# Optimization experiments

Hardware: AMD Instinct MI355X
Metric: run time of the kernel (lower is better)

## Reference

```python
import jax, jax.numpy as jnp
import numpy as np

B, LQ, NB, NT = 4, 512, 32, 256
D_MODEL, N_HEADS, D_K, D_V = 512, 8, 64, 64
SCALE = 1.0 / np.sqrt(D_K).astype(np.float32)


def setup_inputs() -> dict:
    key = jax.random.key(0)
    ks = jax.random.split(key, 16)
    std = 0.02
    p = lambda k, shp: (std * jax.random.normal(k, shp, dtype=jnp.float32))
    return {
        'q':   jax.random.normal(ks[0], (B, LQ, D_MODEL), dtype=jnp.float32),
        'k_w': jax.random.normal(ks[1], (B, NB, NT, D_MODEL), dtype=jnp.float32),
        'v_w': jax.random.normal(ks[2], (B, NB, NT, D_MODEL), dtype=jnp.float32),
        'k_s': jax.random.normal(ks[3], (B, NB, D_MODEL), dtype=jnp.float32),
        'v_s': jax.random.normal(ks[4], (B, NB, D_MODEL), dtype=jnp.float32),
        'W_qs': p(ks[5], (D_MODEL, N_HEADS * D_K)), 'b_qs': jnp.zeros((N_HEADS * D_K,), jnp.float32),
        'W_ks': p(ks[6], (D_MODEL, N_HEADS * D_K)), 'b_ks': jnp.zeros((N_HEADS * D_K,), jnp.float32),
        'W_vs': p(ks[7], (D_MODEL, N_HEADS * D_V)), 'b_vs': jnp.zeros((N_HEADS * D_V,), jnp.float32),
        'W_qw': p(ks[8], (D_MODEL, N_HEADS * D_K)), 'b_qw': jnp.zeros((N_HEADS * D_K,), jnp.float32),
        'W_kw': p(ks[9], (D_MODEL, N_HEADS * D_K)), 'b_kw': jnp.zeros((N_HEADS * D_K,), jnp.float32),
        'W_vw': p(ks[10], (D_MODEL, N_HEADS * D_V)), 'b_vw': jnp.zeros((N_HEADS * D_V,), jnp.float32),
        'W_fc1': p(ks[11], (N_HEADS * D_V, D_MODEL)), 'b_fc1': jnp.zeros((D_MODEL,), jnp.float32),
        'W_fc':  p(ks[12], (D_MODEL + N_HEADS * D_V, D_MODEL)), 'b_fc': jnp.zeros((D_MODEL,), jnp.float32),
    }


def reference(q, k_w, v_w, k_s, v_s,
              W_qs, b_qs, W_ks, b_ks, W_vs, b_vs,
              W_qw, b_qw, W_kw, b_kw, W_vw, b_vw,
              W_fc1, b_fc1, W_fc, b_fc):
    b, lq = q.shape[0], q.shape[1]
    nb, nt = k_w.shape[1], k_w.shape[2]
    h, dk, dv = N_HEADS, D_K, D_V

    # ---- sentence-level (graph) attention ----
    qs = (q @ W_qs + b_qs).reshape(b, lq, h, dk)        # [b,lq,h,dk]
    ks_ = (k_s @ W_ks + b_ks).reshape(b, nb, h, dk)     # [b,nb,h,dk]
    vs_ = (v_s @ W_vs + b_vs).reshape(b, nb, h, dv)     # [b,nb,h,dv]
    attn_s = jnp.einsum('bqhd,bnhd->bhqn', qs * SCALE, ks_)  # [b,h,lq,nb]
    attn_s = jax.nn.softmax(attn_s, axis=-1)
    ctx_s = jnp.einsum('bhqn,bnhd->bqhd', attn_s, vs_).reshape(b, lq, h * dv)
    ctx_s = ctx_s @ W_fc1 + b_fc1                        # [b,lq,d_model]

    # ---- token-level attention with sentence norm ----
    qw = (q @ W_qw + b_qw).reshape(b, lq, h, dk)         # [b,lq,h,dk]
    kw = (k_w @ W_kw + b_kw).reshape(b, nb, nt, h, dk)
    vw = (v_w @ W_vw + b_vw).reshape(b, nb, nt, h, dv)
    attn_w = jnp.einsum('bqhd,bnthd->bhqnt', qw * SCALE, kw)  # [b,h,lq,nb,nt]
    wts = jax.nn.softmax(attn_w, axis=-1)                # softmax over tokens within each block
    aw = wts * attn_s[..., None]                         # sentence-weighted token attention
    ctx_w = jnp.einsum('bhqnt,bnthd->bqhd', aw, vw).reshape(b, lq, h * dv)

    out = jnp.concatenate([ctx_s, ctx_w], axis=-1) @ W_fc + b_fc  # [b,lq,d_model]
    return out
```

## Files before the change

kernel.cpp:

```cpp
#include <hip/hip_runtime.h>
#include <hip/hip_bf16.h>

#define SCALE_F 0.125f

typedef __attribute__((ext_vector_type(8))) short short8;
typedef __attribute__((ext_vector_type(4))) float f32x4;

__device__ __forceinline__ unsigned short f2b(float f){
  return __builtin_bit_cast(unsigned short, __float2bfloat16(f));
}
__device__ __forceinline__ float b2f(unsigned short h){
  return __uint_as_float((unsigned int)h << 16);
}

__global__ __launch_bounds__(256)
void wcast_t(const float* __restrict__ W0, unsigned short* __restrict__ T0,
             const float* __restrict__ W1, unsigned short* __restrict__ T1)
{
  __shared__ unsigned short tile[64][72];
  const float* W = blockIdx.z ? W1 : W0;
  unsigned short* T = blockIdx.z ? T1 : T0;
  int k0 = blockIdx.x * 64, n0 = blockIdx.y * 64;
  #pragma unroll
  for (int j = 0; j < 16; j++) {
    int idx = threadIdx.x + j * 256;
    int r = idx >> 6, c = idx & 63;
    tile[r][c] = f2b(W[(size_t)(k0 + r) * 512 + n0 + c]);
  }
  __syncthreads();
  #pragma unroll
  for (int j = 0; j < 16; j++) {
    int idx = threadIdx.x + j * 256;
    int r = idx >> 6, c = idx & 63;
    T[(size_t)(n0 + r) * 512 + k0 + c] = tile[c][r];
  }
}

template<int MODE>
__device__ __forceinline__ void sgemm_body(
    unsigned short* sm, const float* __restrict__ A,
    const float* __restrict__ p0, const float* __restrict__ p1,
    const float* __restrict__ W, const float* __restrict__ bias,
    float* __restrict__ outf, float scale, int m0, int n0, int K, int tid)
{
  unsigned short* Ah = sm;
  unsigned short* Al = sm + 4096;
  unsigned short* Bh = sm + 8192;
  unsigned short* Bl = sm + 12288;
  const int lane = tid & 63, wv = tid >> 6, lr = lane & 15, lg = lane >> 4;

  f32x4 acc[4];
  #pragma unroll
  for (int nf = 0; nf < 4; nf++) acc[nf] = (f32x4){0.f, 0.f, 0.f, 0.f};

  for (int k0 = 0; k0 < K; k0 += 64) {
    float4 a0[2], a1[2];
    float bw[2][8];
    const bool dual = (MODE == 1) && (k0 >= 512);
    const int kk = dual ? (k0 - 512) : k0;
    #pragma unroll
    for (int j = 0; j < 2; j++) {
      int idx = tid + j * 256;
      int row = idx >> 3, c8 = idx & 7;
      size_t base = (size_t)(m0 + row) * 512 + kk + c8 * 8;
      if (dual) {
        float4 x0 = *(const float4*)&p0[base];
        float4 x1 = *(const float4*)&p0[base + 4];
        float4 y0 = *(const float4*)&p1[base];
        float4 y1 = *(const float4*)&p1[base + 4];
        a0[j] = (float4){x0.x + y0.x, x0.y + y0.y, x0.z + y0.z, x0.w + y0.w};
        a1[j] = (float4){x1.x + y1.x, x1.y + y1.y, x1.z + y1.z, x1.w + y1.w};
      } else {
        a0[j] = *(const float4*)&A[base];
        a1[j] = *(const float4*)&A[base + 4];
      }
    }
    #pragma unroll
    for (int j = 0; j < 2; j++) {
      int idx = tid + j * 256;
      int nl = idx >> 3, kseg = idx & 7;
      #pragma unroll
      for (int e = 0; e < 8; e++)
        bw[j][e] = W[(size_t)(k0 + kseg * 8 + e) * 512 + n0 + nl];
    }
    __syncthreads();
    #pragma unroll
    for (int j = 0; j < 2; j++) {
      int idx = tid + j * 256;
      int row = idx >> 3, c8 = idx & 7;
      int off = row * 64 + ((c8 * 8) ^ ((row & 7) << 3));
      float v[8] = {a0[j].x, a0[j].y, a0[j].z, a0[j].w,
                    a1[j].x, a1[j].y, a1[j].z, a1[j].w};
      short8 h, l;
      #pragma unroll
      for (int e = 0; e < 8; e++) {
        unsigned short hh = f2b(v[e]);
        h[e] = (short)hh;
        l[e] = (short)f2b(v[e] - b2f(hh));
      }
      *(short8*)&Ah[off] = h;
      *(short8*)&Al[off] = l;
    }
    #pragma unroll
    for (int j = 0; j < 2; j++) {
      int idx = tid + j * 256;
      int nl = idx >> 3, kseg = idx & 7;
      int off = nl * 64 + ((kseg * 8) ^ ((nl & 7) << 3));
      short8 h, l;
      #pragma unroll
      for (int e = 0; e < 8; e++) {
        unsigned short hh = f2b(bw[j][e]);
        h[e] = (short)hh;
        l[e] = (short)f2b(bw[j][e] - b2f(hh));
      }
      *(short8*)&Bh[off] = h;
      *(short8*)&Bl[off] = l;
    }
    __syncthreads();
    #pragma unroll
    for (int ks = 0; ks < 2; ks++) {
      int rowa = wv * 16 + lr;
      int aoff = rowa * 64 + ((ks * 32 + lg * 8) ^ ((rowa & 7) << 3));
      short8 ah = *(const short8*)&Ah[aoff];
      short8 al = *(const short8*)&Al[aoff];
      #pragma unroll
      for (int nf = 0; nf < 4; nf++) {
        int rowb = nf * 16 + lr;
        int boff = rowb * 64 + ((ks * 32 + lg * 8) ^ ((rowb & 7) << 3));
        short8 bh = *(const short8*)&Bh[boff];
        short8 bl = *(const short8*)&Bl[boff];
        acc[nf] = __builtin_amdgcn_mfma_f32_16x16x32_bf16(ah, bh, acc[nf], 0, 0, 0);
        acc[nf] = __builtin_amdgcn_mfma_f32_16x16x32_bf16(ah, bl, acc[nf], 0, 0, 0);
        acc[nf] = __builtin_amdgcn_mfma_f32_16x16x32_bf16(al, bh, acc[nf], 0, 0, 0);
      }
    }
  }

  #pragma unroll
  for (int nf = 0; nf < 4; nf++) {
    int n = n0 + nf * 16 + lr;
    float bv = bias[n];
    #pragma unroll
    for (int i = 0; i < 4; i++) {
      int m = m0 + wv * 16 + lg * 4 + i;
      float v = (acc[nf][i] + bv) * scale;
      if (MODE == 0 || MODE == 1) {
        outf[(size_t)m * 512 + n] = v;
      } else if (MODE == 2) {
        int bb = m >> 9, qq = m & 511, hh = n >> 6, d = n & 63;
        outf[((((size_t)bb * 8 + hh) * 512 + qq) << 6) + d] = v;
      } else {
        int bb = m >> 5, nn = m & 31, hh = n >> 6, d = n & 63;
        outf[((((size_t)bb * 8 + hh) * 32 + nn) << 6) + d] = v;
      }
    }
  }
}

template<int VT>
__device__ __forceinline__ void proj_body(
    unsigned short* sm, const float* __restrict__ A,
    const unsigned short* __restrict__ BT, const float* __restrict__ bias,
    __hip_bfloat16* __restrict__ outW, int bidLocal, int tid)
{
  unsigned short* As = sm;
  unsigned short* Bs = sm + 8192;
  const int xcd = bidLocal & 7, local = bidLocal >> 3;
  const int mx = xcd * 32 + (local >> 2);
  const int ny = local & 3;
  const int m0 = mx * 128, n0 = ny * 128;
  const int lane = tid & 63, wv = tid >> 6, lr = lane & 15, lg = lane >> 4;
  const int wr = wv >> 1, wc = wv & 1;

  f32x4 acc[4][4];
  #pragma unroll
  for (int mi = 0; mi < 4; mi++)
    #pragma unroll
    for (int nj = 0; nj < 4; nj++) acc[mi][nj] = (f32x4){0.f, 0.f, 0.f, 0.f};

  for (int k0 = 0; k0 < 512; k0 += 64) {
    float4 a0[4], a1[4]; uint4 bq[4];
    #pragma unroll
    for (int j = 0; j < 4; j++) {
      int idx = tid + j * 256;
      int row = idx >> 3, c8 = idx & 7;
      const float* ap = A + (size_t)(m0 + row) * 512 + k0 + c8 * 8;
      a0[j] = *(const float4*)ap;
      a1[j] = *(const float4*)(ap + 4);
      bq[j] = *(const uint4*)(BT + (size_t)(n0 + row) * 512 + k0 + c8 * 8);
    }
    __syncthreads();
    #pragma unroll
    for (int j = 0; j < 4; j++) {
      int idx = tid + j * 256;
      int row = idx >> 3, c8 = idx & 7;
      int off = row * 64 + ((c8 * 8) ^ ((row & 7) << 3));
      short8 pk;
      pk[0] = (short)f2b(a0[j].x); pk[1] = (short)f2b(a0[j].y);
      pk[2] = (short)f2b(a0[j].z); pk[3] = (short)f2b(a0[j].w);
      pk[4] = (short)f2b(a1[j].x); pk[5] = (short)f2b(a1[j].y);
      pk[6] = (short)f2b(a1[j].z); pk[7] = (short)f2b(a1[j].w);
      *(short8*)&As[off] = pk;
      *(uint4*)&Bs[off] = bq[j];
    }
    __syncthreads();
    #pragma unroll
    for (int ks = 0; ks < 2; ks++) {
      short8 af[4], bfp[4];
      #pragma unroll
      for (int mi = 0; mi < 4; mi++) {
        int row = wr * 64 + mi * 16 + lr;
        af[mi] = *(const short8*)&As[row * 64 + ((ks * 32 + lg * 8) ^ ((row & 7) << 3))];
      }
      #pragma unroll
      for (int nj = 0; nj < 4; nj++) {
        int row = wc * 64 + nj * 16 + lr;
        bfp[nj] = *(const short8*)&Bs[row * 64 + ((ks * 32 + lg * 8) ^ ((row & 7) << 3))];
      }
      #pragma unroll
      for (int mi = 0; mi < 4; mi++)
        #pragma unroll
        for (int nj = 0; nj < 4; nj++)
          acc[mi][nj] = __builtin_amdgcn_mfma_f32_16x16x32_bf16(af[mi], bfp[nj], acc[mi][nj], 0, 0, 0);
    }
  }

  #pragma unroll
  for (int nj = 0; nj < 4; nj++) {
    int n = n0 + wc * 64 + nj * 16 + lr;
    float bv = bias[n];
    int hh = n >> 6, d = n & 63;
    #pragma unroll
    for (int mi = 0; mi < 4; mi++) {
      if (VT == 0) {
        #pragma unroll
        for (int i = 0; i < 4; i++) {
          int m = m0 + wr * 64 + mi * 16 + lg * 4 + i;
          int bb = m >> 13, r = m & 8191, nn = r >> 8, tt = r & 255;
          outW[(((((size_t)bb * 8 + hh) * 32 + nn) * 256 + tt) << 6) + d] =
              __float2bfloat16(acc[mi][nj][i] + bv);
        }
      } else {
        int m = m0 + wr * 64 + mi * 16 + lg * 4;
        int bb = m >> 13, r = m & 8191, nn = r >> 8, t0 = r & 255;
        uint2 pk;
        pk.x = (unsigned)f2b(acc[mi][nj][0] + bv) | ((unsigned)f2b(acc[mi][nj][1] + bv) << 16);
        pk.y = (unsigned)f2b(acc[mi][nj][2] + bv) | ((unsigned)f2b(acc[mi][nj][3] + bv) << 16);
        *(uint2*)((unsigned short*)outW +
                  (((((size_t)bb * 8 + hh) * 32 + nn) * 64 + d) << 8) + t0) = pk;
      }
    }
  }
}

__device__ __forceinline__ void tok_body(
    unsigned short* sm, const float* __restrict__ qw,
    const __hip_bfloat16* __restrict__ kw, const __hip_bfloat16* __restrict__ vwT,
    const float* __restrict__ attn_s, float* __restrict__ part0,
    float* __restrict__ part1, int bid, int tid)
{
  unsigned short* kvbuf = sm;
  unsigned short* pbuf  = sm + 18432;
  const int xcd = bid & 7, slot = bid >> 3;
  const int bh = xcd * 4 + (slot >> 4);
  const int rest = slot & 15;
  const int qt = rest >> 1, z = rest & 1;
  const int b = bh >> 3, h = bh & 7;
  const int wv = tid >> 6, lane = tid & 63, lg = lane >> 4, lr = lane & 15;
  const int qbase = qt * 64 + wv * 16;
  const int n0 = z * 16;
  const int vd = wv * 16 + (lane >> 2), tq = lane & 3;

  short8 qfrag[2];
  {
    const float* qrow = qw + ((size_t)bh * 512 + qbase + lr) * 64;
    #pragma unroll
    for (int ks = 0; ks < 2; ks++) {
      float4 u0 = *(const float4*)&qrow[ks * 32 + lg * 8];
      float4 u1 = *(const float4*)&qrow[ks * 32 + lg * 8 + 4];
      short8 t;
      t[0] = f2b(u0.x); t[1] = f2b(u0.y); t[2] = f2b(u0.z); t[3] = f2b(u0.w);
      t[4] = f2b(u1.x); t[5] = f2b(u1.y); t[6] = f2b(u1.z); t[7] = f2b(u1.w);
      qfrag[ks] = t;
    }
  }
  float asv[16];
  {
    const float* ap = attn_s + ((size_t)bh * 512 + qbase + lr) * 32 + n0;
    #pragma unroll
    for (int i = 0; i < 4; i++) {
      float4 u = *(const float4*)&ap[i * 4];
      asv[i * 4 + 0] = u.x; asv[i * 4 + 1] = u.y;
      asv[i * 4 + 2] = u.z; asv[i * 4 + 3] = u.w;
    }
  }

  f32x4 acc[4];
  #pragma unroll
  for (int dt = 0; dt < 4; dt++) acc[dt] = (f32x4){0.f, 0.f, 0.f, 0.f};

  const unsigned short* kwb = (const unsigned short*)kw + (size_t)bh * 32 * 256 * 64;
  const unsigned short* vtb = (const unsigned short*)vwT + (size_t)bh * 32 * 64 * 256;
  const unsigned int pbase = (wv * 16 + lr) * 264;

  for (int ni = 0; ni < 16; ni++) {
    const int n = n0 + ni;
    __syncthreads();
    {
      const unsigned short* ksrc = kwb + ((size_t)n * 256 + tid) * 64;
      uint4 r[8];
      #pragma unroll
      for (int j = 0; j < 8; j++) r[j] = *(const uint4*)(ksrc + j * 8);
      #pragma unroll
      for (int j = 0; j < 8; j++) *(uint4*)&kvbuf[tid * 72 + j * 8] = r[j];
    }
    __syncthreads();

    f32x4 sfr[16];
    #pragma unroll
    for (int tt = 0; tt < 16; tt++) sfr[tt] = (f32x4){0.f, 0.f, 0.f, 0.f};
    __builtin_amdgcn_s_setprio(1);
    #pragma unroll
    for (int tt = 0; tt < 16; tt++) {
      #pragma unroll
      for (int ks = 0; ks < 2; ks++) {
        short8 kf = *(const short8*)&kvbuf[(16 * tt + lr) * 72 + ks * 32 + lg * 8];
        sfr[tt] = __builtin_amdgcn_mfma_f32_16x16x32_bf16(kf, qfrag[ks], sfr[tt], 0, 0, 0);
      }
    }
    __builtin_amdgcn_s_setprio(0);
    float lsum = 0.f;
    #pragma unroll
    for (int tt = 0; tt < 16; tt++) {
      #pragma unroll
      for (int i = 0; i < 4; i++) {
        float e = __expf(sfr[tt][i]);
        sfr[tt][i] = e;
        lsum += e;
      }
    }
    lsum += __shfl_xor(lsum, 16);
    lsum += __shfl_xor(lsum, 32);
    const float coef = asv[ni] / lsum;
    #pragma unroll
    for (int tt = 0; tt < 16; tt++) {
      uint2 pk;
      pk.x = (unsigned)f2b(sfr[tt][0] * coef) | ((unsigned)f2b(sfr[tt][1] * coef) << 16);
      pk.y = (unsigned)f2b(sfr[tt][2] * coef) | ((unsigned)f2b(sfr[tt][3] * coef) << 16);
      *(uint2*)&pbuf[pbase + tt * 16 + lg * 4] = pk;
    }
    __syncthreads();

    {
      const unsigned short* vsrc = vtb + ((size_t)n * 64 + vd) * 256 + tq * 64;
      uint4 r[8];
      #pragma unroll
      for (int j = 0; j < 8; j++) r[j] = *(const uint4*)(vsrc + j * 8);
      #pragma unroll
      for (int j = 0; j < 8; j++)
        *(uint4*)&kvbuf[vd * 264 + tq * 64 + ((j ^ tq) * 8)] = r[j];
    }
    __syncthreads();

    __builtin_amdgcn_s_setprio(1);
    #pragma unroll
    for (int ks = 0; ks < 8; ks++) {
      short8 pa = *(const short8*)&pbuf[pbase + ks * 32 + lg * 8];
      const int tqe = ks >> 1, joff = (ks & 1) * 4 + lg;
      #pragma unroll
      for (int dt = 0; dt < 4; dt++) {
        short8 vb = *(const short8*)&kvbuf[(16 * dt + lr) * 264 + tqe * 64 + ((joff ^ tqe) * 8)];
        acc[dt] = __builtin_amdgcn_mfma_f32_16x16x32_bf16(pa, vb, acc[dt], 0, 0, 0);
      }
    }
    __builtin_amdgcn_s_setprio(0);
  }

  float* pout = z ? part1 : part0;
  #pragma unroll
  for (int dt = 0; dt < 4; dt++) {
    #pragma unroll
    for (int i = 0; i < 4; i++) {
      int qg = qt * 64 + wv * 16 + lg * 4 + i;
      pout[((size_t)b * 512 + qg) * 512 + h * 64 + dt * 16 + lr] = acc[dt][i];
    }
  }
}

__global__ __launch_bounds__(256)
void megaA(const float* __restrict__ q,
           const float* __restrict__ k_w, const float* __restrict__ v_w,
           const float* __restrict__ k_s, const float* __restrict__ v_s,
           const float* __restrict__ W_qs, const float* __restrict__ b_qs,
           const float* __restrict__ W_qw, const float* __restrict__ b_qw,
           const float* __restrict__ W_ks, const float* __restrict__ b_ks,
           const float* __restrict__ W_vs, const float* __restrict__ b_vs,
           const unsigned short* __restrict__ WkT, const float* __restrict__ b_kw,
           const unsigned short* __restrict__ WvT, const float* __restrict__ b_vw,
           float* qs_ws, float* qw_ws, float* ks_ws, float* vs_ws,
           __hip_bfloat16* kw_ws, __hip_bfloat16* vwT_ws)
{
  __shared__ unsigned short sm[16384];
  const int bid = blockIdx.x, tid = threadIdx.x;
  if (bid < 1024) {
    proj_body<0>(sm, k_w, WkT, b_kw, kw_ws, bid, tid);
  } else if (bid < 2048) {
    proj_body<1>(sm, v_w, WvT, b_vw, vwT_ws, bid - 1024, tid);
  } else if (bid < 2560) {
    int local = bid - 2048;
    int bx = local & 31, by = (local >> 5) & 7, bz = local >> 8;
    if (bz == 0)
      sgemm_body<2>(sm, q, nullptr, nullptr, W_qs, b_qs, qs_ws, SCALE_F, bx * 64, by * 64, 512, tid);
    else
      sgemm_body<2>(sm, q, nullptr, nullptr, W_qw, b_qw, qw_ws, SCALE_F, bx * 64, by * 64, 512, tid);
  } else {
    int local = bid - 2560;
    int bx = local & 1, by = (local >> 1) & 7, bz = local >> 4;
    if (bz == 0)
      sgemm_body<3>(sm, k_s, nullptr, nullptr, W_ks, b_ks, ks_ws, 1.f, bx * 64, by * 64, 512, tid);
    else
      sgemm_body<3>(sm, v_s, nullptr, nullptr, W_vs, b_vs, vs_ws, 1.f, bx * 64, by * 64, 512, tid);
  }
}

__global__ __launch_bounds__(256, 2)
void megaB(const float* __restrict__ qw,
           const __hip_bfloat16* __restrict__ kw, const __hip_bfloat16* __restrict__ vwT,
           const float* __restrict__ attn_s, float* part0, float* part1,
           const float* __restrict__ ctxs,
           const float* __restrict__ W_fc1, const float* __restrict__ b_fc1,
           float* ctxsf)
{
  __shared__ unsigned short sm[35328];
  const int bid = blockIdx.x, tid = threadIdx.x;
  if (bid < 512) {
    tok_body(sm, qw, kw, vwT, attn_s, part0, part1, bid, tid);
  } else {
    int local = bid - 512;
    sgemm_body<0>(sm, ctxs, nullptr, nullptr, W_fc1, b_fc1, ctxsf, 1.f,
                  (local & 31) * 64, (local >> 5) * 64, 512, tid);
  }
}

__global__ __launch_bounds__(256)
void final_gemm(const float* __restrict__ ctxsf,
                const float* __restrict__ p0, const float* __restrict__ p1,
                const float* __restrict__ W, const float* __restrict__ bias,
                float* out)
{
  __shared__ unsigned short sm[16384];
  sgemm_body<1>(sm, ctxsf, p0, p1, W, bias, out, 1.f,
                blockIdx.x * 64, blockIdx.y * 64, 1024, threadIdx.x);
}

__global__ __launch_bounds__(256)
void sent_attn(const float* __restrict__ qs,
               const float* __restrict__ ks,
               const float* __restrict__ vs,
               float* __restrict__ attn_s,
               float* __restrict__ ctx_s)
{
  __shared__ float qsS[32][68];
  __shared__ float ksS[32][68];
  __shared__ float vsS[32][68];
  __shared__ float sS[32][36];
  const int bh = blockIdx.y, b = bh >> 3, h = bh & 7;
  const int q0 = blockIdx.x * 32;
  const int tid = threadIdx.x;

  #pragma unroll
  for (int i = 0; i < 2; i++) {
    int idx = tid + i * 256;
    int r = idx >> 4, c = (idx & 15) * 4;
    *(float4*)&qsS[r][c] = *(const float4*)&qs[((size_t)bh * 512 + q0 + r) * 64 + c];
    *(float4*)&ksS[r][c] = *(const float4*)&ks[((size_t)bh * 32 + r) * 64 + c];
    *(float4*)&vsS[r][c] = *(const float4*)&vs[((size_t)bh * 32 + r) * 64 + c];
  }
  __syncthreads();

  #pragma unroll
  for (int it = 0; it < 4; it++) {
    int pair = tid + it * 256;
    int qq = pair >> 5, nn = pair & 31;
    float s = 0.f;
    #pragma unroll
    for (int k = 0; k < 64; k++) s += qsS[qq][k] * ksS[nn][k];
    sS[qq][nn] = s;
  }
  __syncthreads();

  if (tid < 32) {
    int qq = tid;
    float m = -1e30f;
    #pragma unroll
    for (int n = 0; n < 32; n++) m = fmaxf(m, sS[qq][n]);
    float p[32];
    float sum = 0.f;
    #pragma unroll
    for (int n = 0; n < 32; n++) { p[n] = __expf(sS[qq][n] - m); sum += p[n]; }
    float inv = 1.f / sum;
    #pragma unroll
    for (int n = 0; n < 32; n++) {
      float pv = p[n] * inv;
      sS[qq][n] = pv;
      attn_s[((size_t)bh * 512 + q0 + qq) * 32 + n] = pv;
    }
  }
  __syncthreads();

  #pragma unroll
  for (int it = 0; it < 8; it++) {
    int idx = tid + it * 256;
    int qq = idx >> 6, d = idx & 63;
    float c = 0.f;
    #pragma unroll
    for (int n = 0; n < 32; n++) c += sS[qq][n] * vsS[n][d];
    ctx_s[((size_t)b * 512 + q0 + qq) * 512 + h * 64 + d] = c;
  }
}

extern "C" void kernel_launch(void* const* d_in, const int* in_sizes, int n_in,
                              void* d_out, int out_size, void* d_ws, size_t ws_size,
                              hipStream_t stream)
{
  (void)in_sizes; (void)n_in; (void)out_size; (void)ws_size;
  const float* q    = (const float*)d_in[0];
  const float* k_w  = (const float*)d_in[1];
  const float* v_w  = (const float*)d_in[2];
  const float* k_s  = (const float*)d_in[3];
  const float* v_s  = (const float*)d_in[4];
  const float* W_qs = (const float*)d_in[5];  const float* b_qs = (const float*)d_in[6];
  const float* W_ks = (const float*)d_in[7];  const float* b_ks = (const float*)d_in[8];
  const float* W_vs = (const float*)d_in[9];  const float* b_vs = (const float*)d_in[10];
  const float* W_qw = (const float*)d_in[11]; const float* b_qw = (const float*)d_in[12];
  const float* W_kw = (const float*)d_in[13]; const float* b_kw = (const float*)d_in[14];
  const float* W_vw = (const float*)d_in[15]; const float* b_vw = (const float*)d_in[16];
  const float* W_fc1= (const float*)d_in[17]; const float* b_fc1= (const float*)d_in[18];
  const float* W_fc = (const float*)d_in[19]; const float* b_fc = (const float*)d_in[20];
  float* out = (float*)d_out;

  char* ws = (char*)d_ws;
  const size_t MB = 1ull << 20;
  const size_t KB = 1ull << 10;
  float* qs_ws    = (float*)(ws + 0 * MB);
  float* qw_ws    = (float*)(ws + 4 * MB);
  float* ks_ws    = (float*)(ws + 8 * MB);
  unsigned short* WkT = (unsigned short*)(ws + 8 * MB + 512 * KB);
  float* vs_ws    = (float*)(ws + 9 * MB);
  unsigned short* WvT = (unsigned short*)(ws + 9 * MB + 512 * KB);
  float* attns_ws = (float*)(ws + 10 * MB);
  float* ctxs_ws  = (float*)(ws + 12 * MB);
  float* ctxsf_ws = (float*)(ws + 16 * MB);
  float* part1    = (float*)(ws + 20 * MB);
  __hip_bfloat16* kw_ws  = (__hip_bfloat16*)(ws + 24 * MB);
  __hip_bfloat16* vwT_ws = (__hip_bfloat16*)(ws + 56 * MB);
  float* part0    = (float*)(ws + 0 * MB);

  dim3 blk(256);
  wcast_t<<<dim3(8, 8, 2), blk, 0, stream>>>(W_kw, WkT, W_vw, WvT);
  megaA<<<dim3(2592), blk, 0, stream>>>(
      q, k_w, v_w, k_s, v_s,
      W_qs, b_qs, W_qw, b_qw, W_ks, b_ks, W_vs, b_vs,
      WkT, b_kw, WvT, b_vw,
      qs_ws, qw_ws, ks_ws, vs_ws, kw_ws, vwT_ws);
  sent_attn<<<dim3(16, 32), blk, 0, stream>>>(qs_ws, ks_ws, vs_ws, attns_ws, ctxs_ws);
  megaB<<<dim3(768), blk, 0, stream>>>(
      qw_ws, kw_ws, vwT_ws, attns_ws, part0, part1,
      ctxs_ws, W_fc1, b_fc1, ctxsf_ws);
  final_gemm<<<dim3(32, 8), blk, 0, stream>>>(ctxsf_ws, part0, part1, W_fc, b_fc, out);
}
```

Before: 287.2 us.

## Pre-cast k_w/v_w to bf16 and stage projection tiles via global_load_lds

Adds a prep kernel that converts the large fp32 k_w and v_w tensors to bf16 in workspace, alongside the existing weight transpose-cast. The k/v projection GEMM then loads bf16 tiles straight into swizzled LDS with global_load_lds, skipping the register round-trip and in-loop conversion. The path is chosen only when the workspace holds at least 152 MB, otherwise the old register-staged path runs. It costs an extra full read and write of both 32 MB inputs and still has no double buffering, since it waits on vmcnt(0) every k-step.

```diff
diff --git a/kernel.cpp b/kernel.cpp
--- a/kernel.cpp
+++ b/kernel.cpp
@@ -5,35 +5,14 @@
 
 typedef __attribute__((ext_vector_type(8))) short short8;
 typedef __attribute__((ext_vector_type(4))) float f32x4;
+typedef __attribute__((address_space(3))) void lds_void;
+typedef const __attribute__((address_space(1))) void glb_void;
 
 __device__ __forceinline__ unsigned short f2b(float f){
   return __builtin_bit_cast(unsigned short, __float2bfloat16(f));
 }
 __device__ __forceinline__ float b2f(unsigned short h){
   return __uint_as_float((unsigned int)h << 16);
-}
-
-__global__ __launch_bounds__(256)
-void wcast_t(const float* __restrict__ W0, unsigned short* __restrict__ T0,
-             const float* __restrict__ W1, unsigned short* __restrict__ T1)
-{
-  __shared__ unsigned short tile[64][72];
-  const float* W = blockIdx.z ? W1 : W0;
-  unsigned short* T = blockIdx.z ? T1 : T0;
-  int k0 = blockIdx.x * 64, n0 = blockIdx.y * 64;
-  #pragma unroll
-  for (int j = 0; j < 16; j++) {
-    int idx = threadIdx.x + j * 256;
-    int r = idx >> 6, c = idx & 63;
-    tile[r][c] = f2b(W[(size_t)(k0 + r) * 512 + n0 + c]);
-  }
-  __syncthreads();
-  #pragma unroll
-  for (int j = 0; j < 16; j++) {
-    int idx = threadIdx.x + j * 256;
-    int r = idx >> 6, c = idx & 63;
-    T[(size_t)(n0 + r) * 512 + k0 + c] = tile[c][r];
-  }
 }
 
 template<int MODE>
@@ -158,73 +137,11 @@
 }
 
 template<int VT>
-__device__ __forceinline__ void proj_body(
-    unsigned short* sm, const float* __restrict__ A,
-    const unsigned short* __restrict__ BT, const float* __restrict__ bias,
-    __hip_bfloat16* __restrict__ outW, int bidLocal, int tid)
-{
-  unsigned short* As = sm;
-  unsigned short* Bs = sm + 8192;
-  const int xcd = bidLocal & 7, local = bidLocal >> 3;
-  const int mx = xcd * 32 + (local >> 2);
-  const int ny = local & 3;
-  const int m0 = mx * 128, n0 = ny * 128;
-  const int lane = tid & 63, wv = tid >> 6, lr = lane & 15, lg = lane >> 4;
-  const int wr = wv >> 1, wc = wv & 1;
-
-  f32x4 acc[4][4];
-  #pragma unroll
-  for (int mi = 0; mi < 4; mi++)
-    #pragma unroll
-    for (int nj = 0; nj < 4; nj++) acc[mi][nj] = (f32x4){0.f, 0.f, 0.f, 0.f};
-
-  for (int k0 = 0; k0 < 512; k0 += 64) {
-    float4 a0[4], a1[4]; uint4 bq[4];
-    #pragma unroll
-    for (int j = 0; j < 4; j++) {
-      int idx = tid + j * 256;
-      int row = idx >> 3, c8 = idx & 7;
-      const float* ap = A + (size_t)(m0 + row) * 512 + k0 + c8 * 8;
-      a0[j] = *(const float4*)ap;
-      a1[j] = *(const float4*)(ap + 4);
-      bq[j] = *(const uint4*)(BT + (size_t)(n0 + row) * 512 + k0 + c8 * 8);
-    }
-    __syncthreads();
-    #pragma unroll
-    for (int j = 0; j < 4; j++) {
-      int idx = tid + j * 256;
-      int row = idx >> 3, c8 = idx & 7;
-      int off = row * 64 + ((c8 * 8) ^ ((row & 7) << 3));
-      short8 pk;
-      pk[0] = (short)f2b(a0[j].x); pk[1] = (short)f2b(a0[j].y);
-      pk[2] = (short)f2b(a0[j].z); pk[3] = (short)f2b(a0[j].w);
-      pk[4] = (short)f2b(a1[j].x); pk[5] = (short)f2b(a1[j].y);
-      pk[6] = (short)f2b(a1[j].z); pk[7] = (short)f2b(a1[j].w);
-      *(short8*)&As[off] = pk;
-      *(uint4*)&Bs[off] = bq[j];
-    }
-    __syncthreads();
-    #pragma unroll
-    for (int ks = 0; ks < 2; ks++) {
-      short8 af[4], bfp[4];
-      #pragma unroll
-      for (int mi = 0; mi < 4; mi++) {
-        int row = wr * 64 + mi * 16 + lr;
-        af[mi] = *(const short8*)&As[row * 64 + ((ks * 32 + lg * 8) ^ ((row & 7) << 3))];
-      }
-      #pragma unroll
-      for (int nj = 0; nj < 4; nj++) {
-        int row = wc * 64 + nj * 16 + lr;
-        bfp[nj] = *(const short8*)&Bs[row * 64 + ((ks * 32 + lg * 8) ^ ((row & 7) << 3))];
-      }
-      #pragma unroll
-      for (int mi = 0; mi < 4; mi++)
-        #pragma unroll
-        for (int nj = 0; nj < 4; nj++)
-          acc[mi][nj] = __builtin_amdgcn_mfma_f32_16x16x32_bf16(af[mi], bfp[nj], acc[mi][nj], 0, 0, 0);
-    }
-  }
-
+__device__ __forceinline__ void proj_epilogue(
+    f32x4 (&acc)[4][4], const float* __restrict__ bias,
+    __hip_bfloat16* __restrict__ outW, int m0, int n0,
+    int wr, int wc, int lr, int lg)
+{
   #pragma unroll
   for (int nj = 0; nj < 4; nj++) {
     int n = n0 + wc * 64 + nj * 16 + lr;
@@ -253,6 +170,136 @@
   }
 }
 
+template<int VT>
+__device__ __forceinline__ void proj_reg(
+    unsigned short* sm, const float* __restrict__ A,
+    const unsigned short* __restrict__ BT, const float* __restrict__ bias,
+    __hip_bfloat16* __restrict__ outW, int bidLocal, int tid)
+{
+  unsigned short* As = sm;
+  unsigned short* Bs = sm + 8192;
+  const int xcd = bidLocal & 7, local = bidLocal >> 3;
+  const int mx = xcd * 32 + (local >> 2);
+  const int ny = local & 3;
+  const int m0 = mx * 128, n0 = ny * 128;
+  const int lane = tid & 63, wv = tid >> 6, lr = lane & 15, lg = lane >> 4;
+  const int wr = wv >> 1, wc = wv & 1;
+
+  f32x4 acc[4][4];
+  #pragma unroll
+  for (int mi = 0; mi < 4; mi++)
+    #pragma unroll
+    for (int nj = 0; nj < 4; nj++) acc[mi][nj] = (f32x4){0.f, 0.f, 0.f, 0.f};
+
+  for (int k0 = 0; k0 < 512; k0 += 64) {
+    float4 a0[4], a1[4]; uint4 bq[4];
+    #pragma unroll
+    for (int j = 0; j < 4; j++) {
+      int idx = tid + j * 256;
+      int row = idx >> 3, c8 = idx & 7;
+      const float* ap = A + (size_t)(m0 + row) * 512 + k0 + c8 * 8;
+      a0[j] = *(const float4*)ap;
+      a1[j] = *(const float4*)(ap + 4);
+      bq[j] = *(const uint4*)(BT + (size_t)(n0 + row) * 512 + k0 + c8 * 8);
+    }
+    __syncthreads();
+    #pragma unroll
+    for (int j = 0; j < 4; j++) {
+      int idx = tid + j * 256;
+      int row = idx >> 3, c8 = idx & 7;
+      int off = row * 64 + ((c8 * 8) ^ ((row & 7) << 3));
+      short8 pk;
+      pk[0] = (short)f2b(a0[j].x); pk[1] = (short)f2b(a0[j].y);
+      pk[2] = (short)f2b(a0[j].z); pk[3] = (short)f2b(a0[j].w);
+      pk[4] = (short)f2b(a1[j].x); pk[5] = (short)f2b(a1[j].y);
+      pk[6] = (short)f2b(a1[j].z); pk[7] = (short)f2b(a1[j].w);
+      *(short8*)&As[off] = pk;
+      *(uint4*)&Bs[off] = bq[j];
+    }
+    __syncthreads();
+    #pragma unroll
+    for (int ks = 0; ks < 2; ks++) {
+      short8 af[4], bfp[4];
+      #pragma unroll
+      for (int mi = 0; mi < 4; mi++) {
+        int row = wr * 64 + mi * 16 + lr;
+        af[mi] = *(const short8*)&As[row * 64 + ((ks * 32 + lg * 8) ^ ((row & 7) << 3))];
+      }
+      #pragma unroll
+      for (int nj = 0; nj < 4; nj++) {
+        int row = wc * 64 + nj * 16 + lr;
+        bfp[nj] = *(const short8*)&Bs[row * 64 + ((ks * 32 + lg * 8) ^ ((row & 7) << 3))];
+      }
+      #pragma unroll
+      for (int mi = 0; mi < 4; mi++)
+        #pragma unroll
+        for (int nj = 0; nj < 4; nj++)
+          acc[mi][nj] = __builtin_amdgcn_mfma_f32_16x16x32_bf16(af[mi], bfp[nj], acc[mi][nj], 0, 0, 0);
+    }
+  }
+  proj_epilogue<VT>(acc, bias, outW, m0, n0, wr, wc, lr, lg);
+}
+
+template<int VT>
+__device__ __forceinline__ void proj_glds(
+    unsigned short* sm, const unsigned short* __restrict__ Abf,
+    const unsigned short* __restrict__ BT, const float* __restrict__ bias,
+    __hip_bfloat16* __restrict__ outW, int bidLocal, int tid)
+{
+  unsigned short* As = sm;
+  unsigned short* Bs = sm + 8192;
+  const int xcd = bidLocal & 7, local = bidLocal >> 3;
+  const int mx = xcd * 32 + (local >> 2);
+  const int ny = local & 3;
+  const int m0 = mx * 128, n0 = ny * 128;
+  const int lane = tid & 63, wv = tid >> 6, lr = lane & 15, lg = lane >> 4;
+  const int wr = wv >> 1, wc = wv & 1;
+  const int srow = tid >> 3, scc = tid & 7;
+
+  f32x4 acc[4][4];
+  #pragma unroll
+  for (int mi = 0; mi < 4; mi++)
+    #pragma unroll
+    for (int nj = 0; nj < 4; nj++) acc[mi][nj] = (f32x4){0.f, 0.f, 0.f, 0.f};
+
+  for (int k0 = 0; k0 < 512; k0 += 64) {
+    __syncthreads();
+    #pragma unroll
+    for (int issue = 0; issue < 4; issue++) {
+      int row = issue * 32 + srow;
+      int cs = (scc ^ (row & 7)) * 8;
+      const unsigned short* ga = Abf + (size_t)(m0 + row) * 512 + k0 + cs;
+      const unsigned short* gb = BT  + (size_t)(n0 + row) * 512 + k0 + cs;
+      unsigned short* la = As + issue * 2048 + wv * 512;
+      unsigned short* lb = Bs + issue * 2048 + wv * 512;
+      __builtin_amdgcn_global_load_lds((glb_void*)ga, (lds_void*)la, 16, 0, 0);
+      __builtin_amdgcn_global_load_lds((glb_void*)gb, (lds_void*)lb, 16, 0, 0);
+    }
+    asm volatile("s_waitcnt vmcnt(0)" ::: "memory");
+    __syncthreads();
+    #pragma unroll
+    for (int ks = 0; ks < 2; ks++) {
+      short8 af[4], bfp[4];
+      #pragma unroll
+      for (int mi = 0; mi < 4; mi++) {
+        int row = wr * 64 + mi * 16 + lr;
+        af[mi] = *(const short8*)&As[row * 64 + ((ks * 32 + lg * 8) ^ ((row & 7) << 3))];
+      }
+      #pragma unroll
+      for (int nj = 0; nj < 4; nj++) {
+        int row = wc * 64 + nj * 16 + lr;
+        bfp[nj] = *(const short8*)&Bs[row * 64 + ((ks * 32 + lg * 8) ^ ((row & 7) << 3))];
+      }
+      #pragma unroll
+      for (int mi = 0; mi < 4; mi++)
+        #pragma unroll
+        for (int nj = 0; nj < 4; nj++)
+          acc[mi][nj] = __builtin_amdgcn_mfma_f32_16x16x32_bf16(af[mi], bfp[nj], acc[mi][nj], 0, 0, 0);
+    }
+  }
+  proj_epilogue<VT>(acc, bias, outW, m0, n0, wr, wc, lr, lg);
+}
+
 __device__ __forceinline__ void tok_body(
     unsigned short* sm, const float* __restrict__ qw,
     const __hip_bfloat16* __restrict__ kw, const __hip_bfloat16* __restrict__ vwT,
@@ -388,8 +435,51 @@
 }
 
 __global__ __launch_bounds__(256)
-void megaA(const float* __restrict__ q,
-           const float* __restrict__ k_w, const float* __restrict__ v_w,
+void prep(const float* __restrict__ kwf, const float* __restrict__ vwf,
+          unsigned short* __restrict__ kbf, unsigned short* __restrict__ vbf,
+          const float* __restrict__ W0, unsigned short* __restrict__ T0,
+          const float* __restrict__ W1, unsigned short* __restrict__ T1,
+          int ncast)
+{
+  __shared__ unsigned short tile[64][72];
+  const int bid = blockIdx.x, tid = threadIdx.x;
+  if (bid < 2 * ncast) {
+    const float* src = (bid < ncast) ? kwf : vwf;
+    unsigned short* dst = (bid < ncast) ? kbf : vbf;
+    size_t off = (size_t)((bid < ncast) ? bid : bid - ncast) * 8192;
+    #pragma unroll
+    for (int i = 0; i < 8; i++) {
+      size_t idx = off + ((size_t)i * 256 + tid) * 4;
+      float4 v = *(const float4*)&src[idx];
+      uint2 pk;
+      pk.x = (unsigned)f2b(v.x) | ((unsigned)f2b(v.y) << 16);
+      pk.y = (unsigned)f2b(v.z) | ((unsigned)f2b(v.w) << 16);
+      *(uint2*)&dst[idx] = pk;
+    }
+  } else {
+    int local = bid - 2 * ncast;
+    const float* W = (local >> 6) ? W1 : W0;
+    unsigned short* T = (local >> 6) ? T1 : T0;
+    int k0 = (local & 7) * 64, n0 = ((local >> 3) & 7) * 64;
+    #pragma unroll
+    for (int j = 0; j < 16; j++) {
+      int idx = tid + j * 256;
+      int r = idx >> 6, c = idx & 63;
+      tile[r][c] = f2b(W[(size_t)(k0 + r) * 512 + n0 + c]);
+    }
+    __syncthreads();
+    #pragma unroll
+    for (int j = 0; j < 16; j++) {
+      int idx = tid + j * 256;
+      int r = idx >> 6, c = idx & 63;
+      T[(size_t)(n0 + r) * 512 + k0 + c] = tile[c][r];
+    }
+  }
+}
+
+__global__ __launch_bounds__(256)
+void megaA_glds(const float* __restrict__ q,
+           const unsigned short* __restrict__ kbf, const unsigned short* __restrict__ vbf,
            const float* __restrict__ k_s, const float* __restrict__ v_s,
            const float* __restrict__ W_qs, const float* __restrict__ b_qs,
            const float* __restrict__ W_qw, const float* __restrict__ b_qw,
@@ -403,9 +493,9 @@
   __shared__ unsigned short sm[16384];
   const int bid = blockIdx.x, tid = threadIdx.x;
   if (bid < 1024) {
-    proj_body<0>(sm, k_w, WkT, b_kw, kw_ws, bid, tid);
+    proj_glds<0>(sm, kbf, WkT, b_kw, kw_ws, bid, tid);
   } else if (bid < 2048) {
-    proj_body<1>(sm, v_w, WvT, b_vw, vwT_ws, bid - 1024, tid);
+    proj_glds<1>(sm, vbf, WvT, b_vw, vwT_ws, bid - 1024, tid);
   } else if (bid < 2560) {
     int local = bid - 2048;
     int bx = local & 31, by = (local >> 5) & 7, bz = local >> 8;
@@ -423,6 +513,42 @@
   }
 }
 
+__global__ __launch_bounds__(256)
+void megaA_reg(const float* __restrict__ q,
+           const float* __restrict__ k_w, const float* __restrict__ v_w,
+           const float* __restrict__ k_s, const float* __restrict__ v_s,
+           const float* __restrict__ W_qs, const float* __restrict__ b_qs,
+           const float* __restrict__ W_qw, const float* __restrict__ b_qw,
+           const float* __restrict__ W_ks, const float* __restrict__ b_ks,
+           const float* __restrict__ W_vs, const float* __restrict__ b_vs,
+           const unsigned short* __restrict__ WkT, const float* __restrict__ b_kw,
+           const unsigned short* __restrict__ WvT, const float* __restrict__ b_vw,
+           float* qs_ws, float* qw_ws, float* ks_ws, float* vs_ws,
+           __hip_bfloat16* kw_ws, __hip_bfloat16* vwT_ws)
+{
+  __shared__ unsigned short sm[16384];
+  const int bid = blockIdx.x, tid = threadIdx.x;
+  if (bid < 1024) {
+    proj_reg<0>(sm, k_w, WkT, b_kw, kw_ws, bid, tid);
+  } else if (bid < 2048) {
+    proj_reg<1>(sm, v_w, WvT, b_vw, vwT_ws, bid - 1024, tid);
+  } else if (bid < 2560) {
+    int local = bid - 2048;
+    int bx = local & 31, by = (local >> 5) & 7, bz = local >> 8;
+    if (bz == 0)
+      sgemm_body<2>(sm, q, nullptr, nullptr, W_qs, b_qs, qs_ws, SCALE_F, bx * 64, by * 64, 512, tid);
+    else
+      sgemm_body<2>(sm, q, nullptr, nullptr, W_qw, b_qw, qw_ws, SCALE_F, bx * 64, by * 64, 512, tid);
+  } else {
+    int local = bid - 2560;
+    int bx = local & 1, by = (local >> 1) & 7, bz = local >> 4;
+    if (bz == 0)
+      sgemm_body<3>(sm, k_s, nullptr, nullptr, W_ks, b_ks, ks_ws, 1.f, bx * 64, by * 64, 512, tid);
+    else
+      sgemm_body<3>(sm, v_s, nullptr, nullptr, W_vs, b_vs, vs_ws, 1.f, bx * 64, by * 64, 512, tid);
+  }
+}
+
 __global__ __launch_bounds__(256, 2)
 void megaB(const float* __restrict__ qw,
            const __hip_bfloat16* __restrict__ kw, const __hip_bfloat16* __restrict__ vwT,
@@ -523,7 +649,7 @@
                               void* d_out, int out_size, void* d_ws, size_t ws_size,
                               hipStream_t stream)
 {
-  (void)in_sizes; (void)n_in; (void)out_size; (void)ws_size;
+  (void)in_sizes; (void)n_in; (void)out_size;
   const float* q    = (const float*)d_in[0];
   const float* k_w  = (const float*)d_in[1];
   const float* v_w  = (const float*)d_in[2];
@@ -554,15 +680,29 @@
   float* part1    = (float*)(ws + 20 * MB);
   __hip_bfloat16* kw_ws  = (__hip_bfloat16*)(ws + 24 * MB);
   __hip_bfloat16* vwT_ws = (__hip_bfloat16*)(ws + 56 * MB);
+  unsigned short* kbf = (unsigned short*)(ws + 88 * MB);
+  unsigned short* vbf = (unsigned short*)(ws + 120 * MB);
   float* part0    = (float*)(ws + 0 * MB);
 
+  const bool use_glds = (ws_size >= 152ull * MB);
+  const int ncast = use_glds ? 2048 : 0;
+
   dim3 blk(256);
-  wcast_t<<<dim3(8, 8, 2), blk, 0, stream>>>(W_kw, WkT, W_vw, WvT);
-  megaA<<<dim3(2592), blk, 0, stream>>>(
-      q, k_w, v_w, k_s, v_s,
-      W_qs, b_qs, W_qw, b_qw, W_ks, b_ks, W_vs, b_vs,
-      WkT, b_kw, WvT, b_vw,
-      qs_ws, qw_ws, ks_ws, vs_ws, kw_ws, vwT_ws);
+  prep<<<dim3(2 * ncast + 128), blk, 0, stream>>>(
+      k_w, v_w, kbf, vbf, W_kw, WkT, W_vw, WvT, ncast);
+  if (use_glds) {
+    megaA_glds<<<dim3(2592), blk, 0, stream>>>(
+        q, kbf, vbf, k_s, v_s,
+        W_qs, b_qs, W_qw, b_qw, W_ks, b_ks, W_vs, b_vs,
+        WkT, b_kw, WvT, b_vw,
+        qs_ws, qw_ws, ks_ws, vs_ws, kw_ws, vwT_ws);
+  } else {
+    megaA_reg<<<dim3(2592), blk, 0, stream>>>(
+        q, k_w, v_w, k_s, v_s,
+        W_qs, b_qs, W_qw, b_qw, W_ks, b_ks, W_vs, b_vs,
+        WkT, b_kw, WvT, b_vw,
+        qs_ws, qw_ws, ks_ws, vs_ws, kw_ws, vwT_ws);
+  }
   sent_attn<<<dim3(16, 32), blk, 0, stream>>>(qs_ws, ks_ws, vs_ws, attns_ws, ctxs_ws);
   megaB<<<dim3(768), blk, 0, stream>>>(
       qw_ws, kw_ws, vwT_ws, attns_ws, part0, part1,
```

Result: faster. 271.1 us (-5.6%).
